# Performance work log

Measured on AMD Instinct MI355X. Metric: run time of the kernel, lower is better.

## Reference

```python
import jax, jax.numpy as jnp
import numpy as np

N = 50000      # nodes
E = 600000     # edges
IN = 128       # input_dim
HID = 128      # hidden_dim
OUT = 128      # output_dim
H = 4          # heads
D = OUT // H   # head dim
R = 4          # rel_num
L = 2          # n_layer
M = 10000      # len(idx)
EPS = 1e-5


def setup_inputs() -> dict:
    key = jax.random.key(0)
    ks = jax.random.split(key, 16)
    f = jax.random.normal
    inp = {
        "x": f(ks[0], (N, IN), jnp.float32),
        "proj_w": f(ks[1], (IN, HID), jnp.float32) / np.sqrt(IN).astype(np.float32),
        "proj_b": jnp.zeros((HID,), jnp.float32),
        "bn_gamma": jnp.ones((HID,), jnp.float32),
        "bn_beta": jnp.zeros((HID,), jnp.float32),
        # per-layer HGTConv params (stacked on leading L axis; layer0 in=HID, layer1 in=OUT, equal here)
        "q_w": f(ks[2], (L, HID, OUT), jnp.float32) / np.sqrt(HID).astype(np.float32),
        "q_b": jnp.zeros((L, OUT), jnp.float32),
        "k_w": f(ks[3], (L, HID, OUT), jnp.float32) / np.sqrt(HID).astype(np.float32),
        "k_b": jnp.zeros((L, OUT), jnp.float32),
        "v_w": f(ks[4], (L, HID, OUT), jnp.float32) / np.sqrt(HID).astype(np.float32),
        "v_b": jnp.zeros((L, OUT), jnp.float32),
        "a_w": f(ks[5], (L, OUT, OUT), jnp.float32) / np.sqrt(OUT).astype(np.float32),
        "a_b": jnp.zeros((L, OUT), jnp.float32),
        "skip": jnp.ones((L,), jnp.float32),
        "a_rel": f(ks[6], (L, R, H, D, D), jnp.float32) / np.sqrt(D).astype(np.float32),
        "m_rel": f(ks[7], (L, R, H, D, D), jnp.float32) / np.sqrt(D).astype(np.float32),
        "p_rel": jnp.ones((L, R, H), jnp.float32),
        "edge_index": jax.random.randint(ks[8], (2, E), 0, N, dtype=jnp.int32),
        "edge_type": jax.random.randint(ks[9], (E,), 0, R, dtype=jnp.int32),
        "idx": jax.random.randint(ks[10], (M,), 0, N, dtype=jnp.int32),
    }
    return inp


def _hgt_forward(x, proj_w, proj_b, bn_gamma, bn_beta, q_w, q_b, k_w, k_b, v_w, v_b,
                 a_w, a_b, skip, a_rel, m_rel, p_rel, edge_index, edge_type, idx):
    # proj + BatchNorm1d (training-mode batch statistics, biased variance)
    h = x @ proj_w + proj_b
    mu = h.mean(axis=0)
    var = jnp.mean((h - mu) ** 2, axis=0)
    h = (h - mu) * jax.lax.rsqrt(var + EPS) * bn_gamma + bn_beta

    src, dst = edge_index[0], edge_index[1]          # message from src(j) to dst(i)
    seg = dst * R + edge_type                        # per-(dst, relation) softmax segments
    scale = np.float32(1.0 / np.sqrt(D))

    for l in range(L):
        q = (h @ q_w[l] + q_b[l]).reshape(N, H, D)
        k = (h @ k_w[l] + k_b[l]).reshape(N, H, D)
        v = (h @ v_w[l] + v_b[l]).reshape(N, H, D)
        # relation-specific key/value transforms for every node/relation: [N,R,H,D]
        k_all = jnp.einsum('nhd,rhde->nrhe', k, a_rel[l])
        v_all = jnp.einsum('nhd,rhde->nrhe', v, m_rel[l])
        k_e = k_all[src, edge_type]                  # [E,H,D]
        v_e = v_all[src, edge_type]                  # [E,H,D]
        score = jnp.sum(q[dst] * k_e, axis=-1) * p_rel[l][edge_type] * scale  # [E,H]
        # per-relation segment softmax over incoming edges of each dst node
        smax = jax.ops.segment_max(score, seg, num_segments=N * R)
        e = jnp.exp(score - smax[seg])
        denom = jax.ops.segment_sum(e, seg, num_segments=N * R)
        alpha = e / denom[seg]                        # [E,H]
        out = jax.ops.segment_sum(alpha[..., None] * v_e, dst, num_segments=N)
        out = out.reshape(N, OUT)
        out = jax.nn.gelu(out, approximate=False) @ a_w[l] + a_b[l]
        b = jax.nn.sigmoid(skip[l])                   # learned skip gate
        h = b * out + (1.0 - b) * h                   # dims match -> residual mix
    return h[idx]


def reference(x, proj_w, proj_b, bn_gamma, bn_beta, q_w, q_b, k_w, k_b, v_w, v_b,
              a_w, a_b, skip, a_rel, m_rel, p_rel, edge_index, edge_type, idx):
    return _hgt_forward(x, proj_w, proj_b, bn_gamma, bn_beta, q_w, q_b, k_w, k_b,
                        v_w, v_b, a_w, a_b, skip, a_rel, m_rel, p_rel,
                        edge_index, edge_type, idx)
```

## Files before the change

### kernel.cpp

```cpp
#include <hip/hip_runtime.h>
#include <math.h>

#define NN 50000
#define EE 600000
#define MOUT 10000
#define DEGCAP 384
#define NT4 (NN * 4)

typedef short bf16x8 __attribute__((ext_vector_type(8)));
typedef float f32x4 __attribute__((ext_vector_type(4)));

__device__ __forceinline__ unsigned short f2bf(float x) {
    unsigned int u = __float_as_uint(x);
    u = (u + 0x7FFFu + ((u >> 16) & 1u)) >> 16;
    return (unsigned short)u;
}
__device__ __forceinline__ float bf2f(unsigned int b) {
    return __uint_as_float(b << 16);
}
__device__ __forceinline__ uint4 pack8bf(float4 a, float4 b) {
    uint4 r;
    r.x = (unsigned int)f2bf(a.x) | ((unsigned int)f2bf(a.y) << 16);
    r.y = (unsigned int)f2bf(a.z) | ((unsigned int)f2bf(a.w) << 16);
    r.z = (unsigned int)f2bf(b.x) | ((unsigned int)f2bf(b.y) << 16);
    r.w = (unsigned int)f2bf(b.z) | ((unsigned int)f2bf(b.w) << 16);
    return r;
}

__global__ __launch_bounds__(256) void prep_kernel(
    const float* __restrict__ proj_w, const float* __restrict__ a_w,
    const float* __restrict__ q_w, const float* __restrict__ q_b,
    const float* __restrict__ a_rel,
    const float* __restrict__ k_w, const float* __restrict__ k_b,
    const float* __restrict__ v_w, const float* __restrict__ v_b,
    const float* __restrict__ m_rel, const float* __restrict__ p_rel,
    const int* __restrict__ ei, const int* __restrict__ et,
    unsigned short* __restrict__ wt_pa, unsigned short* __restrict__ qkvw,
    float* __restrict__ fbias, unsigned short* __restrict__ msg_wt,
    int* __restrict__ cnt, int E)
{
    const int b = blockIdx.x, t = threadIdx.x;
    if (b < 192) {
        int wi = b >> 6;
        int flat = (b & 63) * 256 + t;
        int n = flat >> 7, c = flat & 127;
        const float* src = (wi == 0) ? proj_w : (wi == 1) ? a_w : a_w + 16384;
        wt_pa[(size_t)wi * 16384 + n * 128 + c] = f2bf(src[c * 128 + n]);
    } else if (b < 960) {
        int q = b - 192;
        int l = q >= 384 ? 1 : 0;
        int flat = (q - l * 384) * 256 + t;
        int nrow = flat >> 7, c = flat & 127;
        unsigned short* wt = qkvw + (size_t)l * 98304;
        float* fb = fbias + l * 768;
        if (nrow < 512) {
            int r = nrow >> 7, hh = (nrow >> 5) & 3, d = nrow & 31;
            float prl = p_rel[l * 16 + r * 4 + hh] * 0.17677669529663687f;
            const float* qwc = q_w + (size_t)l * 16384 + c * 128 + hh * 32;
            const float* ar  = a_rel + (size_t)(l * 4 + r) * 4096 + hh * 1024 + d * 32;
            float s = 0.f;
            #pragma unroll 8
            for (int e = 0; e < 32; ++e) s += qwc[e] * ar[e];
            wt[(size_t)nrow * 128 + c] = f2bf(s * prl);
            if (c == 0) {
                const float* qb = q_b + l * 128 + hh * 32;
                float bb = 0.f;
                #pragma unroll 8
                for (int e = 0; e < 32; ++e) bb += qb[e] * ar[e];
                fb[nrow] = bb * prl;
            }
        } else {
            int j = nrow - 512;
            int tt = j >> 3, s = j & 7;
            int col = 4 * tt + (s & 3);
            const float* w  = (s < 4) ? k_w : v_w;
            const float* bb = (s < 4) ? k_b : v_b;
            wt[(size_t)nrow * 128 + c] = f2bf(w[(size_t)l * 16384 + c * 128 + col]);
            if (c == 0) fb[nrow] = bb[l * 128 + col];
        }
    } else if (b < 1088) {
        int q = b - 960;
        int l = q >= 64 ? 1 : 0;
        int flat = (q - l * 64) * 256 + t;
        int r = flat >> 12, rem = flat & 4095;
        int n = rem >> 5, d = rem & 31;
        float val = m_rel[(size_t)(l * 4 + r) * 4096 + (n >> 5) * 1024 + d * 32 + (n & 31)];
        msg_wt[(size_t)l * 16384 + r * 4096 + n * 32 + d] = f2bf(val);
    } else {
        int e = (b - 1088) * 256 + t;
        if (e < E) atomicAdd(&cnt[ei[E + e] * 4 + et[e]], 1);
    }
}

__global__ __launch_bounds__(256) void scan_block_kernel(const int* __restrict__ cnt,
    int* __restrict__ excl, int* __restrict__ bsum, int n)
{
    __shared__ int tmp[256];
    int i = blockIdx.x * 256 + threadIdx.x;
    int v = (i < n) ? cnt[i] : 0;
    tmp[threadIdx.x] = v;
    __syncthreads();
    for (int ofs = 1; ofs < 256; ofs <<= 1) {
        int t = (threadIdx.x >= ofs) ? tmp[threadIdx.x - ofs] : 0;
        __syncthreads();
        tmp[threadIdx.x] += t;
        __syncthreads();
    }
    if (i < n) excl[i] = tmp[threadIdx.x] - v;
    if (threadIdx.x == 255) bsum[blockIdx.x] = tmp[255];
}

__global__ __launch_bounds__(256) void scan_add_kernel(int* __restrict__ excl,
    const int* __restrict__ bsum, int* __restrict__ fill,
    int* __restrict__ maskz, int n, int total)
{
    __shared__ int red[256];
    const int b = blockIdx.x;
    int partial = 0;
    for (int j = threadIdx.x; j < b; j += 256) partial += bsum[j];
    red[threadIdx.x] = partial;
    __syncthreads();
    for (int ofs = 128; ofs > 0; ofs >>= 1) {
        if (threadIdx.x < ofs) red[threadIdx.x] += red[threadIdx.x + ofs];
        __syncthreads();
    }
    int prefix = red[0];
    int i = b * 256 + threadIdx.x;
    if (i < n) {
        int o = excl[i] + prefix;
        excl[i] = o;
        fill[i] = o;
    }
    if (i < 12500) maskz[i] = 0;
    if (b == 0 && threadIdx.x == 0) excl[n] = total;
}

__global__ __launch_bounds__(256) void projstats_kernel(
    const float* __restrict__ X, const unsigned short* __restrict__ Wt,
    const float* __restrict__ bias, unsigned short* __restrict__ Cb,
    float* __restrict__ stats, int M,
    const int* __restrict__ ei, const int* __restrict__ et,
    int* __restrict__ fill, int* __restrict__ pack,
    const int* __restrict__ idxp, unsigned char* __restrict__ mask,
    int Mo, int E, int psB)
{
    __shared__ unsigned short As[64 * 136];
    __shared__ unsigned short Bs[128 * 40];
    const int t = threadIdx.x;
    if (blockIdx.x >= psB) {
        int e = (blockIdx.x - psB) * 256 + t;
        if (e < E) {
            int seg = ei[E + e] * 4 + et[e];
            int p = atomicAdd(&fill[seg], 1);
            pack[p] = ei[e];
            if (e < Mo) mask[idxp[e]] = 1;
        }
        return;
    }
    const int wave = t >> 6, lane = t & 63;
    const int quad = lane >> 4, l16 = lane & 15;
    const int row0 = blockIdx.x * 64;
    const int wcl = wave * 32;
    const int sr = t >> 1, scc = (t & 1) * 16;
    const int sr4 = t >> 2, sc4 = (t & 3) * 32;
    const int grow = row0 + sr4;
    const bool rvalid = grow < M;

    f32x4 acc[4][2];
    #pragma unroll
    for (int i = 0; i < 4; ++i)
        #pragma unroll
        for (int j = 0; j < 2; ++j)
            acc[i][j] = (f32x4){0.f, 0.f, 0.f, 0.f};

    uint4 av[4];
    #pragma unroll
    for (int j = 0; j < 4; ++j) av[j] = make_uint4(0, 0, 0, 0);
    if (rvalid) {
        const float4* ap = (const float4*)(X + (size_t)grow * 128 + sc4);
        #pragma unroll
        for (int j = 0; j < 4; ++j) av[j] = pack8bf(ap[2 * j], ap[2 * j + 1]);
    }
    uint4 pv0, pv1;
    {
        const uint4* bp = (const uint4*)(Wt + (size_t)sr * 128 + scc);
        pv0 = bp[0]; pv1 = bp[1];
    }
    for (int it = 0; it < 4; ++it) {
        __syncthreads();
        if (it == 0) {
            #pragma unroll
            for (int j = 0; j < 4; ++j)
                *(uint4*)(As + sr4 * 136 + sc4 + j * 8) = av[j];
        }
        *(uint4*)(Bs + sr * 40 + scc)     = pv0;
        *(uint4*)(Bs + sr * 40 + scc + 8) = pv1;
        __syncthreads();
        if (it + 1 < 4) {
            const uint4* bp = (const uint4*)(Wt + (size_t)sr * 128 + (it + 1) * 32 + scc);
            pv0 = bp[0]; pv1 = bp[1];
        }
        bf16x8 af[4], bfr[2];
        #pragma unroll
        for (int f = 0; f < 4; ++f)
            af[f] = *(const bf16x8*)(As + (f * 16 + l16) * 136 + it * 32 + quad * 8);
        #pragma unroll
        for (int f = 0; f < 2; ++f)
            bfr[f] = *(const bf16x8*)(Bs + (wcl + f * 16 + l16) * 40 + quad * 8);
        #pragma unroll
        for (int fr = 0; fr < 4; ++fr)
            #pragma unroll
            for (int fc = 0; fc < 2; ++fc)
                acc[fr][fc] = __builtin_amdgcn_mfma_f32_16x16x32_bf16(
                    af[fr], bfr[fc], acc[fr][fc], 0, 0, 0);
    }

    #pragma unroll
    for (int fc = 0; fc < 2; ++fc) {
        const int col = wcl + fc * 16 + l16;
        const float bv = bias[col];
        float s = 0.f, s2 = 0.f;
        #pragma unroll
        for (int fr = 0; fr < 4; ++fr)
            #pragma unroll
            for (int reg = 0; reg < 4; ++reg) {
                int row = row0 + fr * 16 + quad * 4 + reg;
                float val = acc[fr][fc][reg] + bv;
                if (row < M) {
                    Cb[(size_t)row * 128 + col] = f2bf(val);
                    s += val; s2 += val * val;
                }
            }
        s  += __shfl_xor(s, 16);  s  += __shfl_xor(s, 32);
        s2 += __shfl_xor(s2, 16); s2 += __shfl_xor(s2, 32);
        if (quad == 0) {
            atomicAdd(&stats[col], s);
            atomicAdd(&stats[128 + col], s2);
        }
    }
}

__global__ __launch_bounds__(256) void bnqkv_kernel(
    const unsigned short* __restrict__ hb, const float* __restrict__ stats,
    const float* __restrict__ gamma, const float* __restrict__ beta,
    const unsigned short* __restrict__ qkvw, const float* __restrict__ fbias,
    unsigned short* __restrict__ hn, unsigned short* __restrict__ qkv, int M)
{
    __shared__ unsigned short hS[128 * 136];
    __shared__ unsigned short Bs[128 * 40];
    __shared__ float mulS[128], addS[128];
    const int t = threadIdx.x;
    const int row0 = blockIdx.x * 128;
    const int ch0 = blockIdx.y * 2;
    if (t < 128) {
        float invN = 1.f / 50000.f;
        float mu = stats[t] * invN;
        float var = stats[128 + t] * invN - mu * mu;
        float ml = rsqrtf(var + 1e-5f) * gamma[t];
        mulS[t] = ml;
        addS[t] = beta[t] - mu * ml;
    }
    __syncthreads();
    #pragma unroll
    for (int u = 0; u < 8; ++u) {
        int li = t + u * 256;
        int row = li >> 4, c0 = (li & 15) * 8;
        uint4 pk = make_uint4(0, 0, 0, 0);
        if (row0 + row < M)
            pk = ((const uint4*)(hb + (size_t)(row0 + row) * 128))[li & 15];
        unsigned int w[4] = {pk.x, pk.y, pk.z, pk.w};
        uint4 o;
        unsigned int ov[4];
        #pragma unroll
        for (int g = 0; g < 4; ++g) {
            int c = c0 + g * 2;
            float a0 = bf2f(w[g] & 0xFFFFu) * mulS[c]     + addS[c];
            float a1 = bf2f(w[g] >> 16)     * mulS[c + 1] + addS[c + 1];
            ov[g] = (unsigned int)f2bf(a0) | ((unsigned int)f2bf(a1) << 16);
        }
        o.x = ov[0]; o.y = ov[1]; o.z = ov[2]; o.w = ov[3];
        *(uint4*)(hS + row * 136 + c0) = o;
        if (blockIdx.y == 0 && row0 + row < M)
            ((uint4*)(hn + (size_t)(row0 + row) * 128))[li & 15] = o;
    }
    __syncthreads();

    const int wave = t >> 6, lane = t & 63;
    const int quad = lane >> 4, l16 = lane & 15;
    const int wr = (wave & 1) * 64, wcl = (wave >> 1) * 64;
    const int sr = t >> 1, scc = (t & 1) * 16;

    uint4 pv0, pv1;
    {
        const uint4* bp = (const uint4*)(qkvw + (size_t)(ch0 * 128 + sr) * 128 + scc);
        pv0 = bp[0]; pv1 = bp[1];
    }
    for (int ch = ch0; ch < ch0 + 2; ++ch) {
        f32x4 acc[4][4];
        #pragma unroll
        for (int i = 0; i < 4; ++i)
            #pragma unroll
            for (int j = 0; j < 4; ++j)
                acc[i][j] = (f32x4){0.f, 0.f, 0.f, 0.f};
        for (int it = 0; it < 4; ++it) {
            __syncthreads();
            *(uint4*)(Bs + sr * 40 + scc)     = pv0;
            *(uint4*)(Bs + sr * 40 + scc + 8) = pv1;
            __syncthreads();
            int nit = it + 1, nch = ch;
            if (nit == 4) { nit = 0; ++nch; }
            if (nch < ch0 + 2) {
                const uint4* bp = (const uint4*)(qkvw + (size_t)(nch * 128 + sr) * 128 + nit * 32 + scc);
                pv0 = bp[0]; pv1 = bp[1];
            }
            bf16x8 af[4], bfr[4];
            #pragma unroll
            for (int f = 0; f < 4; ++f) {
                af[f]  = *(const bf16x8*)(hS + (wr + f * 16 + l16) * 136 + it * 32 + quad * 8);
                bfr[f] = *(const bf16x8*)(Bs + (wcl + f * 16 + l16) * 40 + quad * 8);
            }
            #pragma unroll
            for (int fr = 0; fr < 4; ++fr)
                #pragma unroll
                for (int fc = 0; fc < 4; ++fc)
                    acc[fr][fc] = __builtin_amdgcn_mfma_f32_16x16x32_bf16(
                        af[fr], bfr[fc], acc[fr][fc], 0, 0, 0);
        }
        float b4[4];
        #pragma unroll
        for (int fc = 0; fc < 4; ++fc)
            b4[fc] = fbias[ch * 128 + wcl + fc * 16 + l16];
        #pragma unroll
        for (int fr = 0; fr < 4; ++fr)
            #pragma unroll
            for (int reg = 0; reg < 4; ++reg) {
                int row = row0 + wr + fr * 16 + quad * 4 + reg;
                if (row >= M) continue;
                #pragma unroll
                for (int fc = 0; fc < 4; ++fc) {
                    int col = ch * 128 + wcl + fc * 16 + l16;
                    qkv[(size_t)row * 768 + col] = f2bf(acc[fr][fc][reg] + b4[fc]);
                }
            }
    }
}

__global__ __launch_bounds__(256) void agg_fused_kernel(
    const unsigned short* __restrict__ qkv,
    const unsigned short* __restrict__ qbuf, int qpitch,
    const int* __restrict__ off4, const int* __restrict__ pack,
    const int* __restrict__ rowmap, unsigned short* __restrict__ aggb, int count)
{
    __shared__ int spack[4][DEGCAP];
    const int wv = threadIdx.x >> 6;
    const int lane = threadIdx.x & 63;
    const int l32 = lane & 31;
    const int hi = lane >> 5;
    const int unit = blockIdx.x * 4 + wv;
    if (unit >= count) return;
    const int node = rowmap ? __builtin_amdgcn_readfirstlane(rowmap[unit]) : unit;

    const uint2* qrow = (const uint2*)(qbuf + (size_t)unit * qpitch);
    uint2 quv[4];
    #pragma unroll
    for (int r = 0; r < 4; ++r) quv[r] = qrow[r * 32 + l32];

    int off_r[5];
    #pragma unroll
    for (int i = 0; i < 5; ++i)
        off_r[i] = __builtin_amdgcn_readfirstlane(off4[node * 4 + i]);
    const int beg = off_r[0];
    const int deg = off_r[4] - beg;
    const bool cached = deg <= DEGCAP;

    uint2 outw[4];

    if (deg == 0) {
        #pragma unroll
        for (int r = 0; r < 4; ++r) { outw[r].x = 0u; outw[r].y = 0u; }
    } else if (cached) {
        for (int i = lane; i < deg; i += 64) spack[wv][i] = pack[beg + i];
        asm volatile("s_waitcnt vmcnt(0) lgkmcnt(0)" ::: "memory");

        int rb[4], ren[4];
        #pragma unroll
        for (int r = 0; r < 4; ++r) { rb[r] = off_r[r] - beg; ren[r] = off_r[r + 1] - beg; }

        uint4 kvA[4], kvB[4];
        #pragma unroll
        for (int r = 0; r < 4; ++r) {
            int i0 = rb[r] + hi;     if (i0 >= ren[r]) i0 = ren[r] - 1;  if (i0 < 0) i0 = 0;
            int i1 = rb[r] + 2 + hi; if (i1 >= ren[r]) i1 = ren[r] - 1;  if (i1 < 0) i1 = 0;
            int s0 = spack[wv][i0], s1 = spack[wv][i1];
            kvA[r] = *(const uint4*)(qkv + (size_t)s0 * 768 + 512 + l32 * 8);
            kvB[r] = *(const uint4*)(qkv + (size_t)s1 * 768 + 512 + l32 * 8);
        }

        #pragma unroll
        for (int r = 0; r < 4; ++r) {
            float q0 = bf2f(quv[r].x & 0xFFFFu), q1 = bf2f(quv[r].x >> 16);
            float q2 = bf2f(quv[r].y & 0xFFFFu), q3 = bf2f(quv[r].y >> 16);
            float den = 0.f, a0 = 0.f, a1 = 0.f, a2 = 0.f, a3 = 0.f;

            {
                uint4 kv0 = kvA[r];
                float p = q0 * bf2f(kv0.x & 0xFFFFu) + q1 * bf2f(kv0.x >> 16)
                        + q2 * bf2f(kv0.y & 0xFFFFu) + q3 * bf2f(kv0.y >> 16);
                p += __shfl_xor(p, 1); p += __shfl_xor(p, 2); p += __shfl_xor(p, 4);
                float e = __expf(fminf(fmaxf(p, -80.f), 80.f));
                if (rb[r] + hi >= ren[r]) e = 0.f;
                den += e;
                a0 += e * bf2f(kv0.z & 0xFFFFu); a1 += e * bf2f(kv0.z >> 16);
                a2 += e * bf2f(kv0.w & 0xFFFFu); a3 += e * bf2f(kv0.w >> 16);

                uint4 kv1 = kvB[r];
                p = q0 * bf2f(kv1.x & 0xFFFFu) + q1 * bf2f(kv1.x >> 16)
                  + q2 * bf2f(kv1.y & 0xFFFFu) + q3 * bf2f(kv1.y >> 16);
                p += __shfl_xor(p, 1); p += __shfl_xor(p, 2); p += __shfl_xor(p, 4);
                e = __expf(fminf(fmaxf(p, -80.f), 80.f));
                if (rb[r] + 2 + hi >= ren[r]) e = 0.f;
                den += e;
                a0 += e * bf2f(kv1.z & 0xFFFFu); a1 += e * bf2f(kv1.z >> 16);
                a2 += e * bf2f(kv1.w & 0xFFFFu); a3 += e * bf2f(kv1.w >> 16);
            }

            for (int i = rb[r] + 4; i < ren[r]; i += 4) {
                int i0 = i + hi;      if (i0 >= ren[r]) i0 = ren[r] - 1;
                int i1 = i + 2 + hi;  if (i1 >= ren[r]) i1 = ren[r] - 1;
                int s0 = spack[wv][i0], s1 = spack[wv][i1];
                uint4 kv0 = *(const uint4*)(qkv + (size_t)s0 * 768 + 512 + l32 * 8);
                uint4 kv1 = *(const uint4*)(qkv + (size_t)s1 * 768 + 512 + l32 * 8);
                {
                    float p = q0 * bf2f(kv0.x & 0xFFFFu) + q1 * bf2f(kv0.x >> 16)
                            + q2 * bf2f(kv0.y & 0xFFFFu) + q3 * bf2f(kv0.y >> 16);
                    p += __shfl_xor(p, 1); p += __shfl_xor(p, 2); p += __shfl_xor(p, 4);
                    float e = __expf(fminf(fmaxf(p, -80.f), 80.f));
                    if (i + hi >= ren[r]) e = 0.f;
                    den += e;
                    a0 += e * bf2f(kv0.z & 0xFFFFu); a1 += e * bf2f(kv0.z >> 16);
                    a2 += e * bf2f(kv0.w & 0xFFFFu); a3 += e * bf2f(kv0.w >> 16);
                }
                {
                    float p = q0 * bf2f(kv1.x & 0xFFFFu) + q1 * bf2f(kv1.x >> 16)
                            + q2 * bf2f(kv1.y & 0xFFFFu) + q3 * bf2f(kv1.y >> 16);
                    p += __shfl_xor(p, 1); p += __shfl_xor(p, 2); p += __shfl_xor(p, 4);
                    float e = __expf(fminf(fmaxf(p, -80.f), 80.f));
                    if (i + 2 + hi >= ren[r]) e = 0.f;
                    den += e;
                    a0 += e * bf2f(kv1.z & 0xFFFFu); a1 += e * bf2f(kv1.z >> 16);
                    a2 += e * bf2f(kv1.w & 0xFFFFu); a3 += e * bf2f(kv1.w >> 16);
                }
            }
            den += __shfl_xor(den, 32);
            a0  += __shfl_xor(a0, 32);
            a1  += __shfl_xor(a1, 32);
            a2  += __shfl_xor(a2, 32);
            a3  += __shfl_xor(a3, 32);
            float inv = den > 0.f ? 1.f / den : 0.f;
            outw[r].x = (unsigned int)f2bf(a0 * inv) | ((unsigned int)f2bf(a1 * inv) << 16);
            outw[r].y = (unsigned int)f2bf(a2 * inv) | ((unsigned int)f2bf(a3 * inv) << 16);
        }
    } else {
        #pragma unroll
        for (int r = 0; r < 4; ++r) {
            float q0 = bf2f(quv[r].x & 0xFFFFu), q1 = bf2f(quv[r].x >> 16);
            float q2 = bf2f(quv[r].y & 0xFFFFu), q3 = bf2f(quv[r].y >> 16);
            float den = 0.f, a0 = 0.f, a1 = 0.f, a2 = 0.f, a3 = 0.f;
            const int pe_end = off_r[r + 1];
            for (int pp = off_r[r]; pp < pe_end; pp += 2) {
                int pe = pp + hi; if (pe >= pe_end) pe = pe_end - 1;
                int src = pack[pe];
                uint4 kv = *(const uint4*)(qkv + (size_t)src * 768 + 512 + l32 * 8);
                float p = q0 * bf2f(kv.x & 0xFFFFu) + q1 * bf2f(kv.x >> 16)
                        + q2 * bf2f(kv.y & 0xFFFFu) + q3 * bf2f(kv.y >> 16);
                p += __shfl_xor(p, 1); p += __shfl_xor(p, 2); p += __shfl_xor(p, 4);
                float e = __expf(fminf(fmaxf(p, -80.f), 80.f));
                if (pp + hi >= pe_end) e = 0.f;
                den += e;
                a0 += e * bf2f(kv.z & 0xFFFFu); a1 += e * bf2f(kv.z >> 16);
                a2 += e * bf2f(kv.w & 0xFFFFu); a3 += e * bf2f(kv.w >> 16);
            }
            den += __shfl_xor(den, 32);
            a0  += __shfl_xor(a0, 32);
            a1  += __shfl_xor(a1, 32);
            a2  += __shfl_xor(a2, 32);
            a3  += __shfl_xor(a3, 32);
            float inv = den > 0.f ? 1.f / den : 0.f;
            outw[r].x = (unsigned int)f2bf(a0 * inv) | ((unsigned int)f2bf(a1 * inv) << 16);
            outw[r].y = (unsigned int)f2bf(a2 * inv) | ((unsigned int)f2bf(a3 * inv) << 16);
        }
    }
    if (hi == 0) {
        uint2* op = (uint2*)(aggb + (size_t)unit * 512);
        #pragma unroll
        for (int r = 0; r < 4; ++r) op[r * 32 + l32] = outw[r];
    }
}

__global__ __launch_bounds__(256) void mlpqkv_kernel(
    const unsigned short* __restrict__ A, const unsigned short* __restrict__ W3c,
    const unsigned short* __restrict__ AWt, const float* __restrict__ a_bias,
    const float* __restrict__ skipv, const unsigned short* __restrict__ hres,
    const unsigned short* __restrict__ qkvw1, const float* __restrict__ fbias1,
    const unsigned char* __restrict__ mask,
    unsigned short* __restrict__ h1, unsigned short* __restrict__ qkv, int M)
{
    __shared__ unsigned short Bs[128 * 40];
    __shared__ unsigned short msgS[64 * 136];
    const int t = threadIdx.x;
    const int wave = t >> 6, lane = t & 63;
    const int quad = lane >> 4, l16 = lane & 15;
    const int row0 = blockIdx.x * 64;
    const int wcl = wave * 32;
    const int sr = t >> 1, scc = (t & 1) * 16;
    const int sr4 = t >> 2, sc4 = (t & 3) * 32;
    const int grow = row0 + sr4;
    const bool rvalid = grow < M;

    f32x4 acc[4][2];
    #pragma unroll
    for (int i = 0; i < 4; ++i)
        #pragma unroll
        for (int j = 0; j < 2; ++j)
            acc[i][j] = (f32x4){0.f, 0.f, 0.f, 0.f};

    uint4 av[4];
    #pragma unroll
    for (int j = 0; j < 4; ++j) av[j] = make_uint4(0, 0, 0, 0);
    if (rvalid) {
        const uint4* ap = (const uint4*)(A + (size_t)grow * 512 + sc4);
        #pragma unroll
        for (int j = 0; j < 4; ++j) av[j] = ap[j];
    }
    uint4 bw0, bw1;
    {
        const uint4* bp = (const uint4*)(W3c + sr * 32 + scc);
        bw0 = bp[0]; bw1 = bp[1];
    }
    for (int it = 0; it < 4; ++it) {
        __syncthreads();
        #pragma unroll
        for (int j = 0; j < 4; ++j)
            *(uint4*)(msgS + sr4 * 136 + sc4 + j * 8) = av[j];
        *(uint4*)(Bs + sr * 40 + scc)     = bw0;
        *(uint4*)(Bs + sr * 40 + scc + 8) = bw1;
        __syncthreads();
        if (it + 1 < 4) {
            if (rvalid) {
                const uint4* ap = (const uint4*)(A + (size_t)grow * 512 + (it + 1) * 128 + sc4);
                #pragma unroll
                for (int j = 0; j < 4; ++j) av[j] = ap[j];
            }
            const uint4* bp = (const uint4*)(W3c + (it + 1) * 4096 + sr * 32 + scc);
            bw0 = bp[0]; bw1 = bp[1];
        }
        bf16x8 af[4], bfr[2];
        #pragma unroll
        for (int f = 0; f < 4; ++f)
            af[f] = *(const bf16x8*)(msgS + (f * 16 + l16) * 136 + wave * 32 + quad * 8);
        #pragma unroll
        for (int f = 0; f < 2; ++f)
            bfr[f] = *(const bf16x8*)(Bs + (wcl + f * 16 + l16) * 40 + quad * 8);
        #pragma unroll
        for (int fr = 0; fr < 4; ++fr)
            #pragma unroll
            for (int fc = 0; fc < 2; ++fc)
                acc[fr][fc] = __builtin_amdgcn_mfma_f32_16x16x32_bf16(
                    af[fr], bfr[fc], acc[fr][fc], 0, 0, 0);
    }
    __syncthreads();

    #pragma unroll
    for (int fr = 0; fr < 4; ++fr)
        #pragma unroll
        for (int reg = 0; reg < 4; ++reg) {
            int rl = fr * 16 + quad * 4 + reg;
            #pragma unroll
            for (int fc = 0; fc < 2; ++fc) {
                int col = wcl + fc * 16 + l16;
                float v = acc[fr][fc][reg];
                float gl = 0.5f * v * (1.f + erff(v * 0.70710678118654752f));
                msgS[rl * 136 + col] = f2bf(gl);
            }
        }

    f32x4 acc2[4][2];
    #pragma unroll
    for (int i = 0; i < 4; ++i)
        #pragma unroll
        for (int j = 0; j < 2; ++j)
            acc2[i][j] = (f32x4){0.f, 0.f, 0.f, 0.f};
    uint4 pv0, pv1;
    {
        const uint4* bp = (const uint4*)(AWt + (size_t)sr * 128 + scc);
        pv0 = bp[0]; pv1 = bp[1];
    }
    for (int it = 0; it < 4; ++it) {
        __syncthreads();
        *(uint4*)(Bs + sr * 40 + scc)     = pv0;
        *(uint4*)(Bs + sr * 40 + scc + 8) = pv1;
        __syncthreads();
        if (it + 1 < 4) {
            const uint4* bp = (const uint4*)(AWt + (size_t)sr * 128 + (it + 1) * 32 + scc);
            pv0 = bp[0]; pv1 = bp[1];
        } else {
            const uint4* bp = (const uint4*)(qkvw1 + (size_t)(4 * 128 + sr) * 128 + scc);
            pv0 = bp[0]; pv1 = bp[1];
        }
        bf16x8 af[4], bfr[2];
        #pragma unroll
        for (int f = 0; f < 4; ++f)
            af[f] = *(const bf16x8*)(msgS + (f * 16 + l16) * 136 + it * 32 + quad * 8);
        #pragma unroll
        for (int f = 0; f < 2; ++f)
            bfr[f] = *(const bf16x8*)(Bs + (wcl + f * 16 + l16) * 40 + quad * 8);
        #pragma unroll
        for (int fr = 0; fr < 4; ++fr)
            #pragma unroll
            for (int fc = 0; fc < 2; ++fc)
                acc2[fr][fc] = __builtin_amdgcn_mfma_f32_16x16x32_bf16(
                    af[fr], bfr[fc], acc2[fr][fc], 0, 0, 0);
    }

    const float gate = 1.f / (1.f + __expf(-skipv[0]));
    __syncthreads();
    #pragma unroll
    for (int fr = 0; fr < 4; ++fr)
        #pragma unroll
        for (int reg = 0; reg < 4; ++reg) {
            int rl = fr * 16 + quad * 4 + reg;
            int row = row0 + rl;
            const bool rv = row < M;
            const bool mw = rv && mask[row];
            #pragma unroll
            for (int fc = 0; fc < 2; ++fc) {
                int col = wcl + fc * 16 + l16;
                float val = acc2[fr][fc][reg] + a_bias[col];
                float nv = val;
                if (rv) {
                    unsigned int hu = hres[(size_t)row * 128 + col];
                    nv = gate * val + (1.f - gate) * bf2f(hu);
                    if (mw) h1[(size_t)row * 128 + col] = f2bf(nv);
                }
                msgS[rl * 136 + col] = f2bf(nv);
            }
        }

    for (int ch = 4; ch < 6; ++ch) {
        f32x4 acc3[4][2];
        #pragma unroll
        for (int i = 0; i < 4; ++i)
            #pragma unroll
            for (int j = 0; j < 2; ++j)
                acc3[i][j] = (f32x4){0.f, 0.f, 0.f, 0.f};
        for (int it = 0; it < 4; ++it) {
            __syncthreads();
            *(uint4*)(Bs + sr * 40 + scc)     = pv0;
            *(uint4*)(Bs + sr * 40 + scc + 8) = pv1;
            __syncthreads();
            int nit = it + 1, nch = ch;
            if (nit == 4) { nit = 0; ++nch; }
            if (nch < 6) {
                const uint4* bp = (const uint4*)(qkvw1 + (size_t)(nch * 128 + sr) * 128 + nit * 32 + scc);
                pv0 = bp[0]; pv1 = bp[1];
            }
            bf16x8 af[4], bfr[2];
            #pragma unroll
            for (int f = 0; f < 4; ++f)
                af[f] = *(const bf16x8*)(msgS + (f * 16 + l16) * 136 + it * 32 + quad * 8);
            #pragma unroll
            for (int f = 0; f < 2; ++f)
                bfr[f] = *(const bf16x8*)(Bs + (wcl + f * 16 + l16) * 40 + quad * 8);
            #pragma unroll
            for (int fr = 0; fr < 4; ++fr)
                #pragma unroll
                for (int fc = 0; fc < 2; ++fc)
                    acc3[fr][fc] = __builtin_amdgcn_mfma_f32_16x16x32_bf16(
                        af[fr], bfr[fc], acc3[fr][fc], 0, 0, 0);
        }
        float b2[2];
        #pragma unroll
        for (int fc = 0; fc < 2; ++fc)
            b2[fc] = fbias1[ch * 128 + wcl + fc * 16 + l16];
        #pragma unroll
        for (int fr = 0; fr < 4; ++fr)
            #pragma unroll
            for (int reg = 0; reg < 4; ++reg) {
                int row = row0 + fr * 16 + quad * 4 + reg;
                if (row >= M) continue;
                #pragma unroll
                for (int fc = 0; fc < 2; ++fc) {
                    int col = ch * 128 + wcl + fc * 16 + l16;
                    qkv[(size_t)row * 768 + col] = f2bf(acc3[fr][fc][reg] + b2[fc]);
                }
            }
    }
}

__global__ __launch_bounds__(256) void q1_kernel(
    const unsigned short* __restrict__ h1, const int* __restrict__ idxp,
    const unsigned short* __restrict__ qkvw1, const float* __restrict__ fbias1,
    unsigned short* __restrict__ q1, int M)
{
    __shared__ unsigned short hS[128 * 136];
    __shared__ unsigned short Bs[128 * 40];
    const int t = threadIdx.x;
    const int row0 = blockIdx.x * 128;
    const int ch = blockIdx.y;
    #pragma unroll
    for (int u = 0; u < 8; ++u) {
        int li = t + u * 256;
        int row = li >> 4, c = li & 15;
        uint4 pk = make_uint4(0, 0, 0, 0);
        if (row0 + row < M) {
            int node = idxp[row0 + row];
            pk = ((const uint4*)(h1 + (size_t)node * 128))[c];
        }
        *(uint4*)(hS + row * 136 + c * 8) = pk;
    }
    __syncthreads();

    const int wave = t >> 6, lane = t & 63;
    const int quad = lane >> 4, l16 = lane & 15;
    const int wr = (wave & 1) * 64, wcl = (wave >> 1) * 64;
    const int sr = t >> 1, scc = (t & 1) * 16;
    uint4 pv0, pv1;
    {
        const uint4* bp = (const uint4*)(qkvw1 + (size_t)(ch * 128 + sr) * 128 + scc);
        pv0 = bp[0]; pv1 = bp[1];
    }
    f32x4 acc[4][4];
    #pragma unroll
    for (int i = 0; i < 4; ++i)
        #pragma unroll
        for (int j = 0; j < 4; ++j)
            acc[i][j] = (f32x4){0.f, 0.f, 0.f, 0.f};
    for (int it = 0; it < 4; ++it) {
        __syncthreads();
        *(uint4*)(Bs + sr * 40 + scc)     = pv0;
        *(uint4*)(Bs + sr * 40 + scc + 8) = pv1;
        __syncthreads();
        if (it + 1 < 4) {
            const uint4* bp = (const uint4*)(qkvw1 + (size_t)(ch * 128 + sr) * 128 + (it + 1) * 32 + scc);
            pv0 = bp[0]; pv1 = bp[1];
        }
        bf16x8 af[4], bfr[4];
        #pragma unroll
        for (int f = 0; f < 4; ++f) {
            af[f]  = *(const bf16x8*)(hS + (wr + f * 16 + l16) * 136 + it * 32 + quad * 8);
            bfr[f] = *(const bf16x8*)(Bs + (wcl + f * 16 + l16) * 40 + quad * 8);
        }
        #pragma unroll
        for (int fr = 0; fr < 4; ++fr)
            #pragma unroll
            for (int fc = 0; fc < 4; ++fc)
                acc[fr][fc] = __builtin_amdgcn_mfma_f32_16x16x32_bf16(
                    af[fr], bfr[fc], acc[fr][fc], 0, 0, 0);
    }
    float b4[4];
    #pragma unroll
    for (int fc = 0; fc < 4; ++fc)
        b4[fc] = fbias1[ch * 128 + wcl + fc * 16 + l16];
    #pragma unroll
    for (int fr = 0; fr < 4; ++fr)
        #pragma unroll
        for (int reg = 0; reg < 4; ++reg) {
            int row = row0 + wr + fr * 16 + quad * 4 + reg;
            if (row >= M) continue;
            #pragma unroll
            for (int fc = 0; fc < 4; ++fc) {
                int col = ch * 128 + wcl + fc * 16 + l16;
                q1[(size_t)row * 512 + col] = f2bf(acc[fr][fc][reg] + b4[fc]);
            }
        }
}

__global__ __launch_bounds__(256) void mlp1_kernel(
    const unsigned short* __restrict__ A, const unsigned short* __restrict__ W3c,
    const unsigned short* __restrict__ AWt, const float* __restrict__ a_bias,
    const float* __restrict__ skipv, const unsigned short* __restrict__ hres,
    const int* __restrict__ rowmap, float* __restrict__ out, int M)
{
    __shared__ unsigned short Bs[128 * 40];
    __shared__ unsigned short msgS[64 * 136];
    const int t = threadIdx.x;
    const int wave = t >> 6, lane = t & 63;
    const int quad = lane >> 4, l16 = lane & 15;
    const int row0 = blockIdx.x * 64;
    const int wcl = wave * 32;
    const int sr = t >> 1, scc = (t & 1) * 16;
    const int sr4 = t >> 2, sc4 = (t & 3) * 32;
    const int grow = row0 + sr4;
    const bool rvalid = grow < M;

    f32x4 acc[4][2];
    #pragma unroll
    for (int i = 0; i < 4; ++i)
        #pragma unroll
        for (int j = 0; j < 2; ++j)
            acc[i][j] = (f32x4){0.f, 0.f, 0.f, 0.f};

    uint4 av[4];
    #pragma unroll
    for (int j = 0; j < 4; ++j) av[j] = make_uint4(0, 0, 0, 0);
    if (rvalid) {
        const uint4* ap = (const uint4*)(A + (size_t)grow * 512 + sc4);
        #pragma unroll
        for (int j = 0; j < 4; ++j) av[j] = ap[j];
    }
    uint4 bw0, bw1;
    {
        const uint4* bp = (const uint4*)(W3c + sr * 32 + scc);
        bw0 = bp[0]; bw1 = bp[1];
    }
    for (int it = 0; it < 4; ++it) {
        __syncthreads();
        #pragma unroll
        for (int j = 0; j < 4; ++j)
            *(uint4*)(msgS + sr4 * 136 + sc4 + j * 8) = av[j];
        *(uint4*)(Bs + sr * 40 + scc)     = bw0;
        *(uint4*)(Bs + sr * 40 + scc + 8) = bw1;
        __syncthreads();
        if (it + 1 < 4) {
            if (rvalid) {
                const uint4* ap = (const uint4*)(A + (size_t)grow * 512 + (it + 1) * 128 + sc4);
                #pragma unroll
                for (int j = 0; j < 4; ++j) av[j] = ap[j];
            }
            const uint4* bp = (const uint4*)(W3c + (it + 1) * 4096 + sr * 32 + scc);
            bw0 = bp[0]; bw1 = bp[1];
        }
        bf16x8 af[4], bfr[2];
        #pragma unroll
        for (int f = 0; f < 4; ++f)
            af[f] = *(const bf16x8*)(msgS + (f * 16 + l16) * 136 + wave * 32 + quad * 8);
        #pragma unroll
        for (int f = 0; f < 2; ++f)
            bfr[f] = *(const bf16x8*)(Bs + (wcl + f * 16 + l16) * 40 + quad * 8);
        #pragma unroll
        for (int fr = 0; fr < 4; ++fr)
            #pragma unroll
            for (int fc = 0; fc < 2; ++fc)
                acc[fr][fc] = __builtin_amdgcn_mfma_f32_16x16x32_bf16(
                    af[fr], bfr[fc], acc[fr][fc], 0, 0, 0);
    }
    __syncthreads();

    #pragma unroll
    for (int fr = 0; fr < 4; ++fr)
        #pragma unroll
        for (int reg = 0; reg < 4; ++reg) {
            int rl = fr * 16 + quad * 4 + reg;
            #pragma unroll
            for (int fc = 0; fc < 2; ++fc) {
                int col = wcl + fc * 16 + l16;
                float v = acc[fr][fc][reg];
                float gl = 0.5f * v * (1.f + erff(v * 0.70710678118654752f));
                msgS[rl * 136 + col] = f2bf(gl);
            }
        }

    f32x4 acc2[4][2];
    #pragma unroll
    for (int i = 0; i < 4; ++i)
        #pragma unroll
        for (int j = 0; j < 2; ++j)
            acc2[i][j] = (f32x4){0.f, 0.f, 0.f, 0.f};
    uint4 pv0, pv1;
    {
        const uint4* bp = (const uint4*)(AWt + (size_t)sr * 128 + scc);
        pv0 = bp[0]; pv1 = bp[1];
    }
    for (int it = 0; it < 4; ++it) {
        __syncthreads();
        *(uint4*)(Bs + sr * 40 + scc)     = pv0;
        *(uint4*)(Bs + sr * 40 + scc + 8) = pv1;
        __syncthreads();
        if (it + 1 < 4) {
            const uint4* bp = (const uint4*)(AWt + (size_t)sr * 128 + (it + 1) * 32 + scc);
            pv0 = bp[0]; pv1 = bp[1];
        }
        bf16x8 af[4], bfr[2];
        #pragma unroll
        for (int f = 0; f < 4; ++f)
            af[f] = *(const bf16x8*)(msgS + (f * 16 + l16) * 136 + it * 32 + quad * 8);
        #pragma unroll
        for (int f = 0; f < 2; ++f)
            bfr[f] = *(const bf16x8*)(Bs + (wcl + f * 16 + l16) * 40 + quad * 8);
        #pragma unroll
        for (int fr = 0; fr < 4; ++fr)
            #pragma unroll
            for (int fc = 0; fc < 2; ++fc)
                acc2[fr][fc] = __builtin_amdgcn_mfma_f32_16x16x32_bf16(
                    af[fr], bfr[fc], acc2[fr][fc], 0, 0, 0);
    }

    const float gate = 1.f / (1.f + __expf(-skipv[0]));
    #pragma unroll
    for (int fr = 0; fr < 4; ++fr)
        #pragma unroll
        for (int reg = 0; reg < 4; ++reg) {
            int row = row0 + fr * 16 + quad * 4 + reg;
            if (row >= M) continue;
            int hrow = rowmap[row];
            #pragma unroll
            for (int fc = 0; fc < 2; ++fc) {
                int col = wcl + fc * 16 + l16;
                float val = acc2[fr][fc][reg] + a_bias[col];
                float nv = gate * val + (1.f - gate) * bf2f((unsigned int)hres[(size_t)hrow * 128 + col]);
                out[(size_t)row * 128 + col] = nv;
            }
        }
}

extern "C" void kernel_launch(void* const* d_in, const int* in_sizes, int n_in,
                              void* d_out, int out_size, void* d_ws, size_t ws_size,
                              hipStream_t stream)
{
    const float* x      = (const float*)d_in[0];
    const float* proj_w = (const float*)d_in[1];
    const float* proj_b = (const float*)d_in[2];
    const float* bn_g   = (const float*)d_in[3];
    const float* bn_b   = (const float*)d_in[4];
    const float* q_w    = (const float*)d_in[5];
    const float* q_b    = (const float*)d_in[6];
    const float* k_w    = (const float*)d_in[7];
    const float* k_b    = (const float*)d_in[8];
    const float* v_w    = (const float*)d_in[9];
    const float* v_b    = (const float*)d_in[10];
    const float* a_w    = (const float*)d_in[11];
    const float* a_b    = (const float*)d_in[12];
    const float* skip   = (const float*)d_in[13];
    const float* a_rel  = (const float*)d_in[14];
    const float* m_rel  = (const float*)d_in[15];
    const float* p_rel  = (const float*)d_in[16];
    const int* edge_index = (const int*)d_in[17];
    const int* edge_type  = (const int*)d_in[18];
    const int* idx        = (const int*)d_in[19];
    float* out = (float*)d_out;

    const int N = NN, E = EE;
    float* ws = (float*)d_ws;
    size_t o = 0;
    float* stats  = ws + o;  o += 256;
    float* fbias  = ws + o;  o += 2 * 768;
    int* cnt  = (int*)(ws + o); o += NT4;
    int* off4 = (int*)(ws + o); o += NT4 + 1;
    int* fill = (int*)(ws + o); o += NT4;
    int* bsum = (int*)(ws + o); o += 1024;
    int* pack = (int*)(ws + o); o += E;
    unsigned short* x_bf   = (unsigned short*)(ws + o); o += (size_t)N * 64;
    unsigned short* h_bf   = (unsigned short*)(ws + o); o += (size_t)N * 64;
    unsigned short* hn_bf  = (unsigned short*)(ws + o); o += (size_t)N * 64;
    unsigned short* h1_bf  = (unsigned short*)(ws + o); o += (size_t)N * 64;
    unsigned short* qkv_bf = (unsigned short*)(ws + o); o += (size_t)N * 384;
    unsigned short* agg_bf = (unsigned short*)(ws + o); o += (size_t)N * 256;
    unsigned short* wt_pa  = (unsigned short*)(ws + o); o += 3 * 16384 / 2;
    unsigned short* qkvw   = (unsigned short*)(ws + o); o += 2 * 98304 / 2;
    unsigned short* msg_wt = (unsigned short*)(ws + o); o += 2 * 65536 / 2;

    unsigned char* mask = (unsigned char*)cnt;
    unsigned short* q1 = x_bf;

    const int NB4 = (NT4 + 255) / 256;
    const int EB  = (E + 255) / 256;
    const int PSB = (N + 63) / 64;

    hipMemsetAsync(stats, 0, 256 * sizeof(float), stream);
    hipMemsetAsync(cnt, 0, (size_t)NT4 * sizeof(int), stream);

    prep_kernel<<<1088 + EB, 256, 0, stream>>>(
        proj_w, a_w, q_w, q_b, a_rel, k_w, k_b, v_w, v_b, m_rel, p_rel,
        edge_index, edge_type,
        wt_pa, qkvw, fbias, msg_wt, cnt, E);

    scan_block_kernel<<<NB4, 256, 0, stream>>>(cnt, off4, bsum, NT4);
    scan_add_kernel<<<NB4, 256, 0, stream>>>(off4, bsum, fill, cnt, NT4, E);

    projstats_kernel<<<PSB + EB, 256, 0, stream>>>(x, wt_pa, proj_b, h_bf, stats, N,
                                                   edge_index, edge_type, fill, pack,
                                                   idx, mask, MOUT, E, PSB);

    {
        dim3 grid((N + 127) / 128, 3);
        bnqkv_kernel<<<grid, 256, 0, stream>>>(h_bf, stats, bn_g, bn_b, qkvw, fbias,
                                               hn_bf, qkv_bf, N);
    }

    agg_fused_kernel<<<(N + 3) / 4, 256, 0, stream>>>(qkv_bf, qkv_bf, 768,
                                                      off4, pack, nullptr, agg_bf, N);

    mlpqkv_kernel<<<(N + 63) / 64, 256, 0, stream>>>(agg_bf, msg_wt, wt_pa + 16384, a_b, skip,
                                                     hn_bf, qkvw + 98304, fbias + 768,
                                                     mask, h1_bf, qkv_bf, N);

    {
        dim3 gq((MOUT + 127) / 128, 4);
        q1_kernel<<<gq, 256, 0, stream>>>(h1_bf, idx, qkvw + 98304, fbias + 768, q1, MOUT);
    }

    agg_fused_kernel<<<(MOUT + 3) / 4, 256, 0, stream>>>(qkv_bf, q1, 512,
                                                         off4, pack, idx, agg_bf, MOUT);

    mlp1_kernel<<<(MOUT + 63) / 64, 256, 0, stream>>>(agg_bf, msg_wt + 16384,
                                                      wt_pa + 2 * 16384, a_b + 128,
                                                      skip + 1, h1_bf, idx, out, MOUT);
}
```

Before: 391.4 us.

## Retile bnqkv to 64-row blocks covering all 768 columns; fold stats memset

```diff
diff --git a/kernel.cpp b/kernel.cpp
--- a/kernel.cpp
+++ b/kernel.cpp
@@ -93,9 +93,10 @@
 }
 
 __global__ __launch_bounds__(256) void scan_block_kernel(const int* __restrict__ cnt,
-    int* __restrict__ excl, int* __restrict__ bsum, int n)
+    int* __restrict__ excl, int* __restrict__ bsum, float* __restrict__ stats, int n)
 {
     __shared__ int tmp[256];
+    if (blockIdx.x == 0) stats[threadIdx.x] = 0.f;
     int i = blockIdx.x * 256 + threadIdx.x;
     int v = (i < n) ? cnt[i] : 0;
     tmp[threadIdx.x] = v;
@@ -246,12 +247,11 @@
     const unsigned short* __restrict__ qkvw, const float* __restrict__ fbias,
     unsigned short* __restrict__ hn, unsigned short* __restrict__ qkv, int M)
 {
-    __shared__ unsigned short hS[128 * 136];
+    __shared__ unsigned short hS[64 * 136];
     __shared__ unsigned short Bs[128 * 40];
     __shared__ float mulS[128], addS[128];
     const int t = threadIdx.x;
-    const int row0 = blockIdx.x * 128;
-    const int ch0 = blockIdx.y * 2;
+    const int row0 = blockIdx.x * 64;
     if (t < 128) {
         float invN = 1.f / 50000.f;
         float mu = stats[t] * invN;
@@ -262,7 +262,7 @@
     }
     __syncthreads();
     #pragma unroll
-    for (int u = 0; u < 8; ++u) {
+    for (int u = 0; u < 4; ++u) {
         int li = t + u * 256;
         int row = li >> 4, c0 = (li & 15) * 8;
         uint4 pk = make_uint4(0, 0, 0, 0);
@@ -280,27 +280,27 @@
         }
         o.x = ov[0]; o.y = ov[1]; o.z = ov[2]; o.w = ov[3];
         *(uint4*)(hS + row * 136 + c0) = o;
-        if (blockIdx.y == 0 && row0 + row < M)
+        if (row0 + row < M)
             ((uint4*)(hn + (size_t)(row0 + row) * 128))[li & 15] = o;
     }
     __syncthreads();
 
     const int wave = t >> 6, lane = t & 63;
     const int quad = lane >> 4, l16 = lane & 15;
-    const int wr = (wave & 1) * 64, wcl = (wave >> 1) * 64;
+    const int wcl = wave * 32;
     const int sr = t >> 1, scc = (t & 1) * 16;
 
     uint4 pv0, pv1;
     {
-        const uint4* bp = (const uint4*)(qkvw + (size_t)(ch0 * 128 + sr) * 128 + scc);
+        const uint4* bp = (const uint4*)(qkvw + (size_t)sr * 128 + scc);
         pv0 = bp[0]; pv1 = bp[1];
     }
-    for (int ch = ch0; ch < ch0 + 2; ++ch) {
-        f32x4 acc[4][4];
+    for (int ch = 0; ch < 6; ++ch) {
+        f32x4 acc[4][2];
         #pragma unroll
         for (int i = 0; i < 4; ++i)
             #pragma unroll
-            for (int j = 0; j < 4; ++j)
+            for (int j = 0; j < 2; ++j)
                 acc[i][j] = (f32x4){0.f, 0.f, 0.f, 0.f};
         for (int it = 0; it < 4; ++it) {
             __syncthreads();
@@ -309,37 +309,38 @@
             __syncthreads();
             int nit = it + 1, nch = ch;
             if (nit == 4) { nit = 0; ++nch; }
-            if (nch < ch0 + 2) {
+            if (nch < 6) {
                 const uint4* bp = (const uint4*)(qkvw + (size_t)(nch * 128 + sr) * 128 + nit * 32 + scc);
                 pv0 = bp[0]; pv1 = bp[1];
             }
-            bf16x8 af[4], bfr[4];
-            #pragma unroll
-            for (int f = 0; f < 4; ++f) {
-                af[f]  = *(const bf16x8*)(hS + (wr + f * 16 + l16) * 136 + it * 32 + quad * 8);
+            bf16x8 af[4], bfr[2];
+            #pragma unroll
+            for (int f = 0; f < 4; ++f)
+                af[f] = *(const bf16x8*)(hS + (f * 16 + l16) * 136 + it * 32 + quad * 8);
+            #pragma unroll
+            for (int f = 0; f < 2; ++f)
                 bfr[f] = *(const bf16x8*)(Bs + (wcl + f * 16 + l16) * 40 + quad * 8);
-            }
             #pragma unroll
             for (int fr = 0; fr < 4; ++fr)
                 #pragma unroll
-                for (int fc = 0; fc < 4; ++fc)
+                for (int fc = 0; fc < 2; ++fc)
                     acc[fr][fc] = __builtin_amdgcn_mfma_f32_16x16x32_bf16(
                         af[fr], bfr[fc], acc[fr][fc], 0, 0, 0);
         }
-        float b4[4];
-        #pragma unroll
-        for (int fc = 0; fc < 4; ++fc)
-            b4[fc] = fbias[ch * 128 + wcl + fc * 16 + l16];
+        float b2[2];
+        #pragma unroll
+        for (int fc = 0; fc < 2; ++fc)
+            b2[fc] = fbias[ch * 128 + wcl + fc * 16 + l16];
         #pragma unroll
         for (int fr = 0; fr < 4; ++fr)
             #pragma unroll
             for (int reg = 0; reg < 4; ++reg) {
-                int row = row0 + wr + fr * 16 + quad * 4 + reg;
+                int row = row0 + fr * 16 + quad * 4 + reg;
                 if (row >= M) continue;
                 #pragma unroll
-                for (int fc = 0; fc < 4; ++fc) {
+                for (int fc = 0; fc < 2; ++fc) {
                     int col = ch * 128 + wcl + fc * 16 + l16;
-                    qkv[(size_t)row * 768 + col] = f2bf(acc[fr][fc][reg] + b4[fc]);
+                    qkv[(size_t)row * 768 + col] = f2bf(acc[fr][fc][reg] + b2[fc]);
                 }
             }
     }
@@ -966,7 +967,6 @@
     const int EB  = (E + 255) / 256;
     const int PSB = (N + 63) / 64;
 
-    hipMemsetAsync(stats, 0, 256 * sizeof(float), stream);
     hipMemsetAsync(cnt, 0, (size_t)NT4 * sizeof(int), stream);
 
     prep_kernel<<<1088 + EB, 256, 0, stream>>>(
@@ -974,18 +974,15 @@
         edge_index, edge_type,
         wt_pa, qkvw, fbias, msg_wt, cnt, E);
 
-    scan_block_kernel<<<NB4, 256, 0, stream>>>(cnt, off4, bsum, NT4);
+    scan_block_kernel<<<NB4, 256, 0, stream>>>(cnt, off4, bsum, stats, NT4);
     scan_add_kernel<<<NB4, 256, 0, stream>>>(off4, bsum, fill, cnt, NT4, E);
 
     projstats_kernel<<<PSB + EB, 256, 0, stream>>>(x, wt_pa, proj_b, h_bf, stats, N,
                                                    edge_index, edge_type, fill, pack,
                                                    idx, mask, MOUT, E, PSB);
 
-    {
-        dim3 grid((N + 127) / 128, 3);
-        bnqkv_kernel<<<grid, 256, 0, stream>>>(h_bf, stats, bn_g, bn_b, qkvw, fbias,
-                                               hn_bf, qkv_bf, N);
-    }
+    bnqkv_kernel<<<(N + 63) / 64, 256, 0, stream>>>(h_bf, stats, bn_g, bn_b, qkvw, fbias,
+                                                    hn_bf, qkv_bf, N);
 
     agg_fused_kernel<<<(N + 3) / 4, 256, 0, stream>>>(qkv_bf, qkv_bf, 768,
                                                       off4, pack, nullptr, agg_bf, N);
```

Result: no change. 391.2 us (-0.1%).
